# Optimization experiments

Hardware: AMD Instinct MI355X
Metric: run time of the kernel (lower is better)

Reference implementation:

```python
import jax, jax.numpy as jnp
import numpy as np
from jax import lax

H = 256        # HIDDEN_DIM
H2 = 2 * H     # BiLSTM output dim
L = 100        # MAX_SENTENCE_LENGHT
B = 16
WE = 100       # word embed size
PE = 50        # pos embed size
VOC = 46       # POS_VOCAB_SIZE + 1
IN0 = WE + PE  # lstm layer-0 input dim


def setup_inputs():
    key = jax.random.key(0)
    ks = jax.random.split(key, 20)
    s = 0.05
    inp = {}
    inp["word_embeds"] = jax.random.normal(ks[0], (B, L, WE), jnp.float32)
    inp["pos_idx"] = jax.random.randint(ks[1], (B, L), 0, VOC)
    inp["sen_lens"] = jax.random.randint(ks[2], (B,), 1, L + 1)
    inp["pos_emb"] = jax.random.normal(ks[3], (VOC, PE), jnp.float32) * s
    # LSTM layer 0 (input dim 150), directions stacked on axis 0 (fwd, rev)
    inp["w_ih0"] = jax.random.normal(ks[4], (2, 4 * H, IN0), jnp.float32) * s
    inp["w_hh0"] = jax.random.normal(ks[5], (2, 4 * H, H), jnp.float32) * s
    inp["b_ih0"] = jax.random.normal(ks[6], (2, 4 * H), jnp.float32) * s
    inp["b_hh0"] = jax.random.normal(ks[7], (2, 4 * H), jnp.float32) * s
    # LSTM layers 1-3 (input dim 512): [layer, dir, ...]
    inp["w_ih"] = jax.random.normal(ks[8], (3, 2, 4 * H, H2), jnp.float32) * s
    inp["w_hh"] = jax.random.normal(ks[9], (3, 2, 4 * H, H), jnp.float32) * s
    inp["b_ih"] = jax.random.normal(ks[10], (3, 2, 4 * H), jnp.float32) * s
    inp["b_hh"] = jax.random.normal(ks[11], (3, 2, 4 * H), jnp.float32) * s
    # PosTagFC: Linear(1024,512), Linear(512,128), Linear(128,1)
    inp["W1"] = jax.random.normal(ks[12], (H2, 2 * H2), jnp.float32) * s
    inp["b1"] = jax.random.normal(ks[13], (H2,), jnp.float32) * s
    inp["W2"] = jax.random.normal(ks[14], (H // 2, H2), jnp.float32) * s
    inp["b2"] = jax.random.normal(ks[15], (H // 2,), jnp.float32) * s
    inp["W3"] = jax.random.normal(ks[16], (1, H // 2), jnp.float32) * s
    inp["b3"] = jax.random.normal(ks[17], (1,), jnp.float32) * s
    return inp


def _lstm_dir(x, wi, wh, bi, bh, reverse):
    # x: [B, L, F]; PyTorch gate order i, f, g, o
    gx = jnp.einsum('blf,gf->blg', x, wi) + bi + bh  # [B, L, 4H]
    xs = jnp.swapaxes(gx, 0, 1)                      # [L, B, 4H]
    if reverse:
        xs = xs[::-1]
    h0 = jnp.zeros((x.shape[0], H), x.dtype)
    def step(carry, g):
        h, c = carry
        g = g + h @ wh.T
        i, f, gg, o = jnp.split(g, 4, axis=-1)
        c = jax.nn.sigmoid(f) * c + jax.nn.sigmoid(i) * jnp.tanh(gg)
        h = jax.nn.sigmoid(o) * jnp.tanh(c)
        return (h, c), h
    _, hs = lax.scan(step, (h0, h0), xs)
    hs = jnp.swapaxes(hs, 0, 1)                      # [B, L, H]
    if reverse:
        hs = hs[:, ::-1]
    return hs


def _forward(word_embeds, pos_idx, sen_lens, pos_emb,
             w_ih0, w_hh0, b_ih0, b_hh0, w_ih, w_hh, b_ih, b_hh,
             W1, b1, W2, b2, W3, b3):
    x = jnp.concatenate([word_embeds, pos_emb[pos_idx]], axis=2)  # [B, L, 150]
    # 4-layer bidirectional LSTM (eval mode: inter-layer dropout off)
    fwd = _lstm_dir(x, w_ih0[0], w_hh0[0], b_ih0[0], b_hh0[0], False)
    bwd = _lstm_dir(x, w_ih0[1], w_hh0[1], b_ih0[1], b_hh0[1], True)
    x = jnp.concatenate([fwd, bwd], axis=-1)
    for l in range(3):
        fwd = _lstm_dir(x, w_ih[l, 0], w_hh[l, 0], b_ih[l, 0], b_hh[l, 0], False)
        bwd = _lstm_dir(x, w_ih[l, 1], w_hh[l, 1], b_ih[l, 1], b_hh[l, 1], True)
        x = jnp.concatenate([fwd, bwd], axis=-1)  # [B, L, 512]
    lstm_out = x
    # pairwise scoring: split W1 so we never materialize the 1024-dim concat
    rooted = jnp.concatenate([jnp.zeros((B, 1, H2), x.dtype), lstm_out], axis=1)  # [B, L+1, 512]
    W1a, W1b = W1[:, :H2], W1[:, H2:]
    h_first = lstm_out @ W1a.T          # [B, L, 512]
    h_root = rooted @ W1b.T             # [B, L+1, 512]
    h1 = jax.nn.relu(h_first[:, :, None, :] + h_root[:, None, :, :] + b1)  # [B, L, L+1, 512]
    h2 = jax.nn.relu(h1 @ W2.T + b2)    # [B, L, L+1, 128]
    sc = (h2 @ W3.T + b3)[..., 0]       # [B, L, L+1]
    # fill_diagonal_ on the [N,1] fc output zeroes only element 0 -> (0,0)
    sc = sc.at[:, 0, 0].set(0.0)
    row_ok = jnp.arange(L)[None, :] < sen_lens[:, None]        # [B, L]
    col_ok = jnp.arange(L + 1)[None, :] <= sen_lens[:, None]   # [B, L+1]
    sc = jnp.where(row_ok[:, :, None] & col_ok[:, None, :], sc, 0.0)
    return jnp.pad(sc, ((0, 0), (0, 1), (0, 0)))  # [B, 101, 101]


def reference(word_embeds, pos_idx, sen_lens, pos_emb,
              w_ih0, w_hh0, b_ih0, b_hh0, w_ih, w_hh, b_ih, b_hh,
              W1, b1, W2, b2, W3, b3):
    return _forward(word_embeds, pos_idx, sen_lens, pos_emb,
                    w_ih0, w_hh0, b_ih0, b_hh0, w_ih, w_hh, b_ih, b_hh,
                    W1, b1, W2, b2, W3, b3)
```

## Files before the change

### kernel.cpp

```cpp
#include <hip/hip_runtime.h>
#include <stdint.h>

#define NB 16
#define NL 100
#define NOUT (16*101*101)

typedef _Float16 f16x8 __attribute__((ext_vector_type(8)));
typedef float f32x4 __attribute__((ext_vector_type(4)));

__device__ __forceinline__ float sigm(float x) {
    x = fminf(fmaxf(x, -30.f), 30.f);
    return 1.f / (1.f + __expf(-x));
}
__device__ __forceinline__ float tanh_(float x) {
    x = fminf(fmaxf(x, -15.f), 15.f);
    float t = __expf(2.f * x);
    return (t - 1.f) / (t + 1.f);
}
__device__ __forceinline__ uint32_t pack2h(_Float16 a, _Float16 b) {
    return (uint32_t)__builtin_bit_cast(uint16_t, a) |
           ((uint32_t)__builtin_bit_cast(uint16_t, b) << 16);
}


__global__ __launch_bounds__(256) void pack_whh_mfma(const float* __restrict__ w_hh0,
                                                     const float* __restrict__ w_hh,
                                                     uint32_t* __restrict__ wpk) {
    int idx = blockIdx.x * 256 + threadIdx.x;
    if (idx >= 262144) return;
    int l6 = idx & 63;
    int kc = (idx >> 6) & 7;
    int mt = (idx >> 9) & 63;
    int ld = idx >> 15;
    int layer = ld >> 1, d = ld & 1;
    int row = mt * 16 + (l6 & 15);
    int k0 = kc * 32 + (l6 >> 4) * 8;
    const float* src = (layer == 0)
        ? &w_hh0[((size_t)d * 1024 + row) * 256]
        : &w_hh[(((size_t)(layer - 1) * 2 + d) * 1024 + row) * 256];
    uint4 o;
    o.x = pack2h((_Float16)src[k0 + 0], (_Float16)src[k0 + 1]);
    o.y = pack2h((_Float16)src[k0 + 2], (_Float16)src[k0 + 3]);
    o.z = pack2h((_Float16)src[k0 + 4], (_Float16)src[k0 + 5]);
    o.w = pack2h((_Float16)src[k0 + 6], (_Float16)src[k0 + 7]);
    *(uint4*)&wpk[(size_t)idx * 4] = o;
}

__global__ __launch_bounds__(256) void pack_w2_mfma(const float* __restrict__ W2,
                                                    uint32_t* __restrict__ w2pk) {
    int idx = blockIdx.x * 256 + threadIdx.x;
    if (idx >= 16384) return;
    int l6 = idx & 63;
    int nt = (idx >> 6) & 7;
    int sp = (idx >> 9) & 1;
    int kc = idx >> 10;
    int ch = nt * 16 + (l6 & 15);
    int k0 = kc * 32 + (l6 >> 4) * 8;
    uint32_t dw[4];
#pragma unroll
    for (int dwi = 0; dwi < 4; ++dwi) {
        float x0 = W2[(size_t)ch * 512 + k0 + dwi * 2 + 0];
        float x1 = W2[(size_t)ch * 512 + k0 + dwi * 2 + 1];
        _Float16 h0 = (_Float16)x0, h1 = (_Float16)x1;
        _Float16 v0 = sp ? (_Float16)(x0 - (float)h0) : h0;
        _Float16 v1 = sp ? (_Float16)(x1 - (float)h1) : h1;
        dw[dwi] = pack2h(v0, v1);
    }
    *(uint4*)&w2pk[(size_t)idx * 4] = make_uint4(dw[0], dw[1], dw[2], dw[3]);
}

__global__ __launch_bounds__(256) void pack_wi0(const float* __restrict__ w_ih0,
                                                float* __restrict__ wi0p) {
    int idx = blockIdx.x * 256 + threadIdx.x;
    if (idx >= 2 * 1024 * 160) return;
    int k = idx % 160;
    int g = (idx / 160) & 1023;
    int d = idx / (160 * 1024);
    float v = (k < 150) ? w_ih0[((size_t)d * 1024 + g) * 150 + k] : 0.f;
    wi0p[idx] = v;
}

__global__ __launch_bounds__(256) void pack_bias(const float* __restrict__ b_ih0,
                                                 const float* __restrict__ b_hh0,
                                                 const float* __restrict__ b_ih,
                                                 const float* __restrict__ b_hh,
                                                 float* __restrict__ biasp) {
    int idx = blockIdx.x * 256 + threadIdx.x;
    if (idx >= 8 * 1024) return;
    int g = idx & 1023;
    int ld = idx >> 10;
    int l = ld >> 1, d = ld & 1;
    float v;
    if (l == 0) v = b_ih0[d * 1024 + g] + b_hh0[d * 1024 + g];
    else {
        size_t o = ((size_t)(l - 1) * 2 + d) * 1024 + g;
        v = b_ih[o] + b_hh[o];
    }
    biasp[idx] = v;
}

__global__ __launch_bounds__(256) void concat_x0(const float* __restrict__ we,
                                                 const int* __restrict__ pos_idx,
                                                 const float* __restrict__ pos_emb,
                                                 float* __restrict__ x0p) {
    int idx = blockIdx.x * 256 + threadIdx.x;
    if (idx >= 1600 * 160) return;
    int m = idx / 160, k = idx % 160;
    float v;
    if (k < 100) v = we[(size_t)m * 100 + k];
    else if (k < 150) v = pos_emb[(size_t)pos_idx[m] * 50 + (k - 100)];
    else v = 0.f;
    x0p[idx] = v;
}

__global__ __launch_bounds__(256) void zero_out(float* __restrict__ out) {
    int idx = blockIdx.x * 256 + threadIdx.x;
    if (idx < NOUT) out[idx] = 0.f;
}

__global__ __launch_bounds__(256) void gemm_xwT(const float* __restrict__ X,
                                                const float* __restrict__ W,
                                                const float* __restrict__ bias,
                                                float* __restrict__ C,
                                                int K, int ldx, int ldw, int ldc, int coff) {
    __shared__ float As[16][68];
    __shared__ float Bs[16][68];
    const int t = threadIdx.x;
    const int m0 = blockIdx.x * 64, n0 = blockIdx.y * 64;
    const int lr = t >> 2, lc = (t & 3) * 4;
    const int tm = (t & 15) * 4, tn = (t >> 4) * 4;
    float acc[4][4] = {};
    for (int kc = 0; kc < K; kc += 16) {
        float4 av = *(const float4*)&X[(size_t)(m0 + lr) * ldx + kc + lc];
        float4 bv = *(const float4*)&W[(size_t)(n0 + lr) * ldw + kc + lc];
        __syncthreads();
        As[lc + 0][lr] = av.x; As[lc + 1][lr] = av.y; As[lc + 2][lr] = av.z; As[lc + 3][lr] = av.w;
        Bs[lc + 0][lr] = bv.x; Bs[lc + 1][lr] = bv.y; Bs[lc + 2][lr] = bv.z; Bs[lc + 3][lr] = bv.w;
        __syncthreads();
#pragma unroll
        for (int k = 0; k < 16; ++k) {
            float4 a = *(const float4*)&As[k][tm];
            float4 b = *(const float4*)&Bs[k][tn];
            acc[0][0] = fmaf(a.x, b.x, acc[0][0]);
            acc[0][1] = fmaf(a.x, b.y, acc[0][1]);
            acc[0][2] = fmaf(a.x, b.z, acc[0][2]);
            acc[0][3] = fmaf(a.x, b.w, acc[0][3]);
            acc[1][0] = fmaf(a.y, b.x, acc[1][0]);
            acc[1][1] = fmaf(a.y, b.y, acc[1][1]);
            acc[1][2] = fmaf(a.y, b.z, acc[1][2]);
            acc[1][3] = fmaf(a.y, b.w, acc[1][3]);
            acc[2][0] = fmaf(a.z, b.x, acc[2][0]);
            acc[2][1] = fmaf(a.z, b.y, acc[2][1]);
            acc[2][2] = fmaf(a.z, b.z, acc[2][2]);
            acc[2][3] = fmaf(a.z, b.w, acc[2][3]);
            acc[3][0] = fmaf(a.w, b.x, acc[3][0]);
            acc[3][1] = fmaf(a.w, b.y, acc[3][1]);
            acc[3][2] = fmaf(a.w, b.z, acc[3][2]);
            acc[3][3] = fmaf(a.w, b.w, acc[3][3]);
        }
    }
#pragma unroll
    for (int r = 0; r < 4; ++r) {
#pragma unroll
        for (int c = 0; c < 4; ++c) {
            float v = acc[r][c];
            if (bias) v += bias[n0 + tn + c];
            C[(size_t)(m0 + tm + r) * ldc + coff + n0 + tn + c] = v;
        }
    }
}

__global__ __launch_bounds__(1024, 4) void lstm_mfma(const float* __restrict__ gx,
                                                     const uint32_t* __restrict__ wpk_layer,
                                                     float* __restrict__ xout) {
    extern __shared__ uint32_t smem[];
    uint32_t* wtail = smem;
    float*    gbuf  = (float*)(smem + 36864);
    uint32_t* hsta  = smem + 37888;

    const int d = blockIdx.x >> 4;
    const int b = blockIdx.x & 15;
    const int t = threadIdx.x;
    const int w = t >> 6;
    const int l = t & 63;
    const int cgrp = l >> 4;

    uint4 wreg[23];
    const uint32_t* wsrc = wpk_layer + (((size_t)d * 64 + w * 4) * 8) * 256;
#pragma unroll
    for (int mtl = 0; mtl < 4; ++mtl)
#pragma unroll
        for (int kc = 0; kc < 8; ++kc) {
            int f = mtl * 8 + kc;
            uint4 v = *(const uint4*)&wsrc[((size_t)mtl * 8 + kc) * 256 + l * 4];
            if (f < 23) wreg[f] = v;
            else *(uint4*)&wtail[((w * 9 + (f - 23)) * 64 + l) * 4] = v;
        }
    if (t < 128) hsta[t] = 0u;
    float creg = 0.f;
    float gxi = 0.f, gxf = 0.f, gxg = 0.f, gxo = 0.f;
    const float* gxb = gx + ((size_t)d * 1600 + b * 100) * 1024;
    if (t < 256) {
        int tt0 = d ? NL - 1 : 0;
        gxi = gxb[(size_t)tt0 * 1024 + t];
        gxf = gxb[(size_t)tt0 * 1024 + 256 + t];
        gxg = gxb[(size_t)tt0 * 1024 + 512 + t];
        gxo = gxb[(size_t)tt0 * 1024 + 768 + t];
    }
    __syncthreads();

    for (int s = 0; s < NL; ++s) {
        const int tt = d ? (NL - 1 - s) : s;
        f32x4 acc0 = {0.f, 0.f, 0.f, 0.f};
        f32x4 acc1 = {0.f, 0.f, 0.f, 0.f};
        f32x4 acc2 = {0.f, 0.f, 0.f, 0.f};
        f32x4 acc3 = {0.f, 0.f, 0.f, 0.f};
#pragma unroll
        for (int kc = 0; kc < 8; ++kc) {
            uint4 braw = *(const uint4*)&hsta[kc * 16 + cgrp * 4];
            f16x8 B = __builtin_bit_cast(f16x8, braw);
            acc0 = __builtin_amdgcn_mfma_f32_16x16x32_f16(
                __builtin_bit_cast(f16x8, wreg[kc]), B, acc0, 0, 0, 0);
            acc1 = __builtin_amdgcn_mfma_f32_16x16x32_f16(
                __builtin_bit_cast(f16x8, wreg[8 + kc]), B, acc1, 0, 0, 0);
            uint4 a2raw = (kc < 7) ? wreg[16 + kc]
                                   : *(const uint4*)&wtail[((w * 9 + 0) * 64 + l) * 4];
            acc2 = __builtin_amdgcn_mfma_f32_16x16x32_f16(
                __builtin_bit_cast(f16x8, a2raw), B, acc2, 0, 0, 0);
            uint4 a3raw = *(const uint4*)&wtail[((w * 9 + kc + 1) * 64 + l) * 4];
            acc3 = __builtin_amdgcn_mfma_f32_16x16x32_f16(
                __builtin_bit_cast(f16x8, a3raw), B, acc3, 0, 0, 0);
        }
        if ((l & 15) == 0) {
            *(f32x4*)&gbuf[w * 64 +  0 + cgrp * 4] = acc0;
            *(f32x4*)&gbuf[w * 64 + 16 + cgrp * 4] = acc1;
            *(f32x4*)&gbuf[w * 64 + 32 + cgrp * 4] = acc2;
            *(f32x4*)&gbuf[w * 64 + 48 + cgrp * 4] = acc3;
        }
        __syncthreads();
        if (t < 256) {
            float gi = gbuf[t] + gxi;
            float gf = gbuf[256 + t] + gxf;
            float gg = gbuf[512 + t] + gxg;
            float go = gbuf[768 + t] + gxo;
            float cn = fmaf(sigm(gf), creg, sigm(gi) * tanh_(gg));
            creg = cn;
            float hn = sigm(go) * tanh_(cn);
            ((_Float16*)hsta)[t] = (_Float16)hn;
            xout[((size_t)b * NL + tt) * 512 + d * 256 + t] = hn;
            if (s + 1 < NL) {
                int tn = d ? (NL - 2 - s) : (s + 1);
                gxi = gxb[(size_t)tn * 1024 + t];
                gxf = gxb[(size_t)tn * 1024 + 256 + t];
                gxg = gxb[(size_t)tn * 1024 + 512 + t];
                gxo = gxb[(size_t)tn * 1024 + 768 + t];
            }
        }
        __syncthreads();
    }
}

__global__ __launch_bounds__(256) void scorer_mfma(const float* __restrict__ hfr,
                                                   const uint32_t* __restrict__ w2pk,
                                                   const float* __restrict__ b1,
                                                   const float* __restrict__ b2,
                                                   const float* __restrict__ W3,
                                                   const float* __restrict__ b3,
                                                   const int* __restrict__ sen_lens,
                                                   float* __restrict__ out) {
    extern __shared__ uint32_t smem[];
    float*    hfs = (float*)smem;
    float*    hrs = hfs + 16 * 520;
    float*    b1s = hrs + 8 * 520;
    uint32_t* w2s = (uint32_t*)(b1s + 512);

    const int t = threadIdx.x;
    const int wv = t >> 6, l = t & 63;
    const int cgrp = l >> 4;
    const int b = blockIdx.z;
    const int i0 = blockIdx.x * 16;
    const int j0 = blockIdx.y * 8;

#pragma unroll
    for (int rep = 0; rep < 8; ++rep) {
        int slot = rep * 256 + t;
        int row = slot >> 7, c4 = slot & 127;
        int i = i0 + row;
        float4 v = make_float4(0.f, 0.f, 0.f, 0.f);
        if (i < 100) v = *(const float4*)&hfr[((size_t)b * 100 + i) * 1024 + c4 * 4];
        *(float4*)&hfs[row * 520 + c4 * 4] = v;
    }
#pragma unroll
    for (int rep = 0; rep < 4; ++rep) {
        int slot = rep * 256 + t;
        int row = slot >> 7, c4 = slot & 127;
        int j = j0 + row;
        float4 v = make_float4(0.f, 0.f, 0.f, 0.f);
        if (j >= 1 && j <= 100)
            v = *(const float4*)&hfr[((size_t)b * 100 + (j - 1)) * 1024 + 512 + c4 * 4];
        *(float4*)&hrs[row * 520 + c4 * 4] = v;
    }
    if (t < 128) *(float4*)&b1s[t * 4] = *(const float4*)&b1[t * 4];

    float b2r[8], w3r[8];
#pragma unroll
    for (int nt = 0; nt < 8; ++nt) {
        b2r[nt] = b2[nt * 16 + (l & 15)];
        w3r[nt] = W3[nt * 16 + (l & 15)];
    }
    f32x4 accA[8], accB[8];
#pragma unroll
    for (int nt = 0; nt < 8; ++nt) {
        accA[nt] = (f32x4){0.f, 0.f, 0.f, 0.f};
        accB[nt] = (f32x4){0.f, 0.f, 0.f, 0.f};
    }
    const int p0 = (wv * 2) * 16 + (l & 15);
    const int p1 = (wv * 2 + 1) * 16 + (l & 15);
    const int ilA = p0 >> 3, jlA = p0 & 7;
    const int ilB = p1 >> 3, jlB = p1 & 7;
    __syncthreads();

    for (int kc = 0; kc < 16; ++kc) {
#pragma unroll
        for (int rep = 0; rep < 4; ++rep) {
            int slot = rep * 256 + t;
            *(uint4*)&w2s[slot * 4] = *(const uint4*)&w2pk[((size_t)kc * 1024 + slot) * 4];
        }
        __syncthreads();
        const int k0 = kc * 32 + cgrp * 8;
        f16x8 ahi0, alo0, ahi1, alo1;
        {
            const float* hf = &hfs[ilA * 520 + k0];
            const float* hr = &hrs[jlA * 520 + k0];
            const float* bb = &b1s[k0];
#pragma unroll
            for (int j = 0; j < 8; ++j) {
                float v = fmaxf(hf[j] + hr[j] + bb[j], 0.f);
                _Float16 hi = (_Float16)v;
                ahi0[j] = hi;
                alo0[j] = (_Float16)(v - (float)hi);
            }
        }
        {
            const float* hf = &hfs[ilB * 520 + k0];
            const float* hr = &hrs[jlB * 520 + k0];
            const float* bb = &b1s[k0];
#pragma unroll
            for (int j = 0; j < 8; ++j) {
                float v = fmaxf(hf[j] + hr[j] + bb[j], 0.f);
                _Float16 hi = (_Float16)v;
                ahi1[j] = hi;
                alo1[j] = (_Float16)(v - (float)hi);
            }
        }
#pragma unroll
        for (int nt = 0; nt < 8; ++nt) {
            f16x8 bhi = __builtin_bit_cast(f16x8, *(const uint4*)&w2s[((0 * 8 + nt) * 64 + l) * 4]);
            f16x8 blo = __builtin_bit_cast(f16x8, *(const uint4*)&w2s[((1 * 8 + nt) * 64 + l) * 4]);
            accA[nt] = __builtin_amdgcn_mfma_f32_16x16x32_f16(ahi0, bhi, accA[nt], 0, 0, 0);
            accA[nt] = __builtin_amdgcn_mfma_f32_16x16x32_f16(ahi0, blo, accA[nt], 0, 0, 0);
            accA[nt] = __builtin_amdgcn_mfma_f32_16x16x32_f16(alo0, bhi, accA[nt], 0, 0, 0);
            accB[nt] = __builtin_amdgcn_mfma_f32_16x16x32_f16(ahi1, bhi, accB[nt], 0, 0, 0);
            accB[nt] = __builtin_amdgcn_mfma_f32_16x16x32_f16(ahi1, blo, accB[nt], 0, 0, 0);
            accB[nt] = __builtin_amdgcn_mfma_f32_16x16x32_f16(alo1, bhi, accB[nt], 0, 0, 0);
        }
        __syncthreads();
    }
    float sp0[4] = {0.f, 0.f, 0.f, 0.f};
    float sp1[4] = {0.f, 0.f, 0.f, 0.f};
#pragma unroll
    for (int nt = 0; nt < 8; ++nt)
#pragma unroll
        for (int r = 0; r < 4; ++r) {
            sp0[r] += fmaxf(accA[nt][r] + b2r[nt], 0.f) * w3r[nt];
            sp1[r] += fmaxf(accB[nt][r] + b2r[nt], 0.f) * w3r[nt];
        }
#pragma unroll
    for (int r = 0; r < 4; ++r) {
#pragma unroll
        for (int off = 1; off < 16; off <<= 1) {
            sp0[r] += __shfl_xor(sp0[r], off);
            sp1[r] += __shfl_xor(sp1[r], off);
        }
    }
    if ((l & 15) == 0) {
        float bias3 = b3[0];
        int sl = sen_lens[b];
#pragma unroll
        for (int mtl = 0; mtl < 2; ++mtl)
#pragma unroll
            for (int r = 0; r < 4; ++r) {
                int p = (wv * 2 + mtl) * 16 + cgrp * 4 + r;
                int i = i0 + (p >> 3), j = j0 + (p & 7);
                if (i < 100 && j < 101) {
                    float v = (mtl == 0 ? sp0[r] : sp1[r]) + bias3;
                    if (!((i < sl) && (j <= sl)) || (i == 0 && j == 0)) v = 0.f;
                    out[((size_t)b * 101 + i) * 101 + j] = v;
                }
            }
    }
}

extern "C" void kernel_launch(void* const* d_in, const int* in_sizes, int n_in,
                              void* d_out, int out_size, void* d_ws, size_t ws_size,
                              hipStream_t stream) {
    const float* we       = (const float*)d_in[0];
    const int*   pos_idx  = (const int*)d_in[1];
    const int*   sen_lens = (const int*)d_in[2];
    const float* pos_emb  = (const float*)d_in[3];
    const float* w_ih0    = (const float*)d_in[4];
    const float* w_hh0    = (const float*)d_in[5];
    const float* b_ih0    = (const float*)d_in[6];
    const float* b_hh0    = (const float*)d_in[7];
    const float* w_ih     = (const float*)d_in[8];
    const float* w_hh     = (const float*)d_in[9];
    const float* b_ih     = (const float*)d_in[10];
    const float* b_hh     = (const float*)d_in[11];
    const float* W1       = (const float*)d_in[12];
    const float* b1       = (const float*)d_in[13];
    const float* W2       = (const float*)d_in[14];
    const float* b2       = (const float*)d_in[15];
    const float* W3       = (const float*)d_in[16];
    const float* b3       = (const float*)d_in[17];
    float* out = (float*)d_out;

    float* ws    = (float*)d_ws;
    float* x0p   = ws;
    float* gx    = x0p + 256000;
    float* xA    = gx + 3276800;
    float* xB    = xA + 819200;
    float* hfr   = xB + 819200;
    float* wi0p  = hfr + 1638400;
    float* biasp = wi0p + 327680;
    uint32_t* wpk  = (uint32_t*)(biasp + 8192);
    uint32_t* w2pk = wpk + 1048576;

    pack_whh_mfma<<<1024, 256, 0, stream>>>(w_hh0, w_hh, wpk);
    pack_w2_mfma<<<64, 256, 0, stream>>>(W2, w2pk);
    pack_wi0<<<1280, 256, 0, stream>>>(w_ih0, wi0p);
    pack_bias<<<32, 256, 0, stream>>>(b_ih0, b_hh0, b_ih, b_hh, biasp);
    concat_x0<<<1000, 256, 0, stream>>>(we, pos_idx, pos_emb, x0p);

    const int LSTM_SMEM = 38016 * 4;
    const int SCOR_SMEM = 68352;

    for (int d = 0; d < 2; ++d)
        gemm_xwT<<<dim3(25, 16), 256, 0, stream>>>(
            x0p, wi0p + (size_t)d * 1024 * 160, biasp + d * 1024,
            gx + (size_t)d * 1600 * 1024, 160, 160, 160, 1024, 0);
    lstm_mfma<<<32, 1024, LSTM_SMEM, stream>>>(gx, wpk, xA);

    const float* xin = xA;
    float* xo = xB;
    for (int l = 1; l < 4; ++l) {
        for (int d = 0; d < 2; ++d)
            gemm_xwT<<<dim3(25, 16), 256, 0, stream>>>(
                xin, w_ih + (((size_t)(l - 1) * 2 + d) * 1024) * 512,
                biasp + (l * 2 + d) * 1024,
                gx + (size_t)d * 1600 * 1024, 512, 512, 512, 1024, 0);
        lstm_mfma<<<32, 1024, LSTM_SMEM, stream>>>(gx, wpk + (size_t)l * 262144, xo);
        float* tmp = (float*)xin; xin = xo; xo = tmp;
    }
    const float* lstm_out = xin;

    gemm_xwT<<<dim3(25, 8), 256, 0, stream>>>(lstm_out, W1, nullptr, hfr,
                                              512, 512, 1024, 1024, 0);
    gemm_xwT<<<dim3(25, 8), 256, 0, stream>>>(lstm_out, W1 + 512, nullptr, hfr,
                                              512, 512, 1024, 1024, 512);

    zero_out<<<(NOUT + 255) / 256, 256, 0, stream>>>(out);
    scorer_mfma<<<dim3(7, 13, 16), 256, SCOR_SMEM, stream>>>(hfr, w2pk, b1, b2, W3, b3,
                                                             sen_lens, out);
}
```

Baseline: 1.205 ms.

## Restructure LSTM recurrence so each wave owns full gate sets; stream W2 from global

```diff
diff --git a/kernel.cpp b/kernel.cpp
--- a/kernel.cpp
+++ b/kernel.cpp
@@ -21,6 +21,8 @@
     return (uint32_t)__builtin_bit_cast(uint16_t, a) |
            ((uint32_t)__builtin_bit_cast(uint16_t, b) << 16);
 }
+#define MFMA16(A, B, C) __builtin_amdgcn_mfma_f32_16x16x32_f16( \
+    __builtin_bit_cast(f16x8, A), (B), (C), 0, 0, 0)
 
 
 __global__ __launch_bounds__(256) void pack_whh_mfma(const float* __restrict__ w_hh0,
@@ -170,109 +172,134 @@
     }
 }
 
-__global__ __launch_bounds__(1024, 4) void lstm_mfma(const float* __restrict__ gx,
-                                                     const uint32_t* __restrict__ wpk_layer,
-                                                     float* __restrict__ xout) {
-    extern __shared__ uint32_t smem[];
-    uint32_t* wtail = smem;
-    float*    gbuf  = (float*)(smem + 36864);
-    uint32_t* hsta  = smem + 37888;
-
+__global__ __launch_bounds__(512, 2) void lstm_v5(const float* __restrict__ gx,
+                                                  const uint32_t* __restrict__ wpk_layer,
+                                                  float* __restrict__ xout) {
+    __shared__ uint32_t hs2[256];
     const int d = blockIdx.x >> 4;
     const int b = blockIdx.x & 15;
     const int t = threadIdx.x;
     const int w = t >> 6;
     const int l = t & 63;
-    const int cgrp = l >> 4;
-
-    uint4 wreg[23];
-    const uint32_t* wsrc = wpk_layer + (((size_t)d * 64 + w * 4) * 8) * 256;
-#pragma unroll
-    for (int mtl = 0; mtl < 4; ++mtl)
-#pragma unroll
-        for (int kc = 0; kc < 8; ++kc) {
-            int f = mtl * 8 + kc;
-            uint4 v = *(const uint4*)&wsrc[((size_t)mtl * 8 + kc) * 256 + l * 4];
-            if (f < 23) wreg[f] = v;
-            else *(uint4*)&wtail[((w * 9 + (f - 23)) * 64 + l) * 4] = v;
-        }
-    if (t < 128) hsta[t] = 0u;
-    float creg = 0.f;
-    float gxi = 0.f, gxf = 0.f, gxg = 0.f, gxo = 0.f;
+    const int lg = l >> 4;
+
+    const uint32_t* wb = wpk_layer + (size_t)d * 131072;
+#define WFRAG(mt, kc) (*(const uint4*)&wb[(((mt) * 8 + (kc)) * 64 + l) * 4])
+
+    uint4 wr0[16], wr1[16];
+#pragma unroll
+    for (int kc = 0; kc < 8; ++kc) {
+#pragma unroll
+        for (int s = 0; s < 2; ++s) {
+            wr0[kc * 2 + s] = WFRAG(w * 2 + s, kc);
+            wr1[kc * 2 + s] = WFRAG(16 + w * 2 + s, kc);
+        }
+    }
+    if (t < 128) hs2[t] = 0u;
+    f32x4 c0 = {0.f, 0.f, 0.f, 0.f}, c1 = {0.f, 0.f, 0.f, 0.f};
+    __syncthreads();
+
     const float* gxb = gx + ((size_t)d * 1600 + b * 100) * 1024;
-    if (t < 256) {
-        int tt0 = d ? NL - 1 : 0;
-        gxi = gxb[(size_t)tt0 * 1024 + t];
-        gxf = gxb[(size_t)tt0 * 1024 + 256 + t];
-        gxg = gxb[(size_t)tt0 * 1024 + 512 + t];
-        gxo = gxb[(size_t)tt0 * 1024 + 768 + t];
-    }
-    __syncthreads();
-
+    const int gxoff = w * 32 + lg * 4;
+
+#pragma unroll 1
     for (int s = 0; s < NL; ++s) {
         const int tt = d ? (NL - 1 - s) : s;
-        f32x4 acc0 = {0.f, 0.f, 0.f, 0.f};
-        f32x4 acc1 = {0.f, 0.f, 0.f, 0.f};
-        f32x4 acc2 = {0.f, 0.f, 0.f, 0.f};
-        f32x4 acc3 = {0.f, 0.f, 0.f, 0.f};
+        const uint32_t* hc = hs2 + (s & 1) * 128;
+        uint32_t* hn = hs2 + ((s + 1) & 1) * 128;
+
+        f32x4 a00 = {0.f,0.f,0.f,0.f}, a01 = {0.f,0.f,0.f,0.f};
+        f32x4 a10 = {0.f,0.f,0.f,0.f}, a11 = {0.f,0.f,0.f,0.f};
+        f32x4 a20 = {0.f,0.f,0.f,0.f}, a21 = {0.f,0.f,0.f,0.f};
+        f32x4 a30 = {0.f,0.f,0.f,0.f}, a31 = {0.f,0.f,0.f,0.f};
+
+        uint4 sr[2][4];
+#pragma unroll
+        for (int p = 0; p < 2; ++p) {
+            sr[p][0] = WFRAG(32 + w * 2 + 0, p);
+            sr[p][1] = WFRAG(32 + w * 2 + 1, p);
+            sr[p][2] = WFRAG(48 + w * 2 + 0, p);
+            sr[p][3] = WFRAG(48 + w * 2 + 1, p);
+        }
+        f32x4 gxv[8];
+
 #pragma unroll
         for (int kc = 0; kc < 8; ++kc) {
-            uint4 braw = *(const uint4*)&hsta[kc * 16 + cgrp * 4];
+            uint4 braw = *(const uint4*)&hc[kc * 16 + lg * 4];
             f16x8 B = __builtin_bit_cast(f16x8, braw);
-            acc0 = __builtin_amdgcn_mfma_f32_16x16x32_f16(
-                __builtin_bit_cast(f16x8, wreg[kc]), B, acc0, 0, 0, 0);
-            acc1 = __builtin_amdgcn_mfma_f32_16x16x32_f16(
-                __builtin_bit_cast(f16x8, wreg[8 + kc]), B, acc1, 0, 0, 0);
-            uint4 a2raw = (kc < 7) ? wreg[16 + kc]
-                                   : *(const uint4*)&wtail[((w * 9 + 0) * 64 + l) * 4];
-            acc2 = __builtin_amdgcn_mfma_f32_16x16x32_f16(
-                __builtin_bit_cast(f16x8, a2raw), B, acc2, 0, 0, 0);
-            uint4 a3raw = *(const uint4*)&wtail[((w * 9 + kc + 1) * 64 + l) * 4];
-            acc3 = __builtin_amdgcn_mfma_f32_16x16x32_f16(
-                __builtin_bit_cast(f16x8, a3raw), B, acc3, 0, 0, 0);
+            a00 = MFMA16(wr0[kc * 2 + 0], B, a00);
+            a01 = MFMA16(wr0[kc * 2 + 1], B, a01);
+            a10 = MFMA16(wr1[kc * 2 + 0], B, a10);
+            a11 = MFMA16(wr1[kc * 2 + 1], B, a11);
+            uint4 s0 = sr[kc & 1][0], s1 = sr[kc & 1][1];
+            uint4 s2 = sr[kc & 1][2], s3 = sr[kc & 1][3];
+            if (kc < 6) {
+                const int p = kc + 2;
+                sr[kc & 1][0] = WFRAG(32 + w * 2 + 0, p);
+                sr[kc & 1][1] = WFRAG(32 + w * 2 + 1, p);
+                sr[kc & 1][2] = WFRAG(48 + w * 2 + 0, p);
+                sr[kc & 1][3] = WFRAG(48 + w * 2 + 1, p);
+            }
+            if (kc == 6) {
+#pragma unroll
+                for (int g = 0; g < 4; ++g)
+#pragma unroll
+                    for (int si = 0; si < 2; ++si)
+                        gxv[g * 2 + si] = *(const f32x4*)&gxb[(size_t)tt * 1024 +
+                                                              g * 256 + si * 16 + gxoff];
+            }
+            a20 = MFMA16(s0, B, a20);
+            a21 = MFMA16(s1, B, a21);
+            a30 = MFMA16(s2, B, a30);
+            a31 = MFMA16(s3, B, a31);
+        }
+
+        float h0[4], h1[4];
+#pragma unroll
+        for (int r = 0; r < 4; ++r) {
+            float gi = a00[r] + gxv[0][r];
+            float gf = a10[r] + gxv[2][r];
+            float gg = a20[r] + gxv[4][r];
+            float go = a30[r] + gxv[6][r];
+            float cn = fmaf(sigm(gf), c0[r], sigm(gi) * tanh_(gg));
+            c0[r] = cn;
+            h0[r] = sigm(go) * tanh_(cn);
+            gi = a01[r] + gxv[1][r];
+            gf = a11[r] + gxv[3][r];
+            gg = a21[r] + gxv[5][r];
+            go = a31[r] + gxv[7][r];
+            cn = fmaf(sigm(gf), c1[r], sigm(gi) * tanh_(gg));
+            c1[r] = cn;
+            h1[r] = sigm(go) * tanh_(cn);
         }
         if ((l & 15) == 0) {
-            *(f32x4*)&gbuf[w * 64 +  0 + cgrp * 4] = acc0;
-            *(f32x4*)&gbuf[w * 64 + 16 + cgrp * 4] = acc1;
-            *(f32x4*)&gbuf[w * 64 + 32 + cgrp * 4] = acc2;
-            *(f32x4*)&gbuf[w * 64 + 48 + cgrp * 4] = acc3;
+            const int u0 = w * 32 + lg * 4;
+            uint2 p0, p1;
+            p0.x = pack2h((_Float16)h0[0], (_Float16)h0[1]);
+            p0.y = pack2h((_Float16)h0[2], (_Float16)h0[3]);
+            p1.x = pack2h((_Float16)h1[0], (_Float16)h1[1]);
+            p1.y = pack2h((_Float16)h1[2], (_Float16)h1[3]);
+            *(uint2*)((char*)hn + (size_t)u0 * 2) = p0;
+            *(uint2*)((char*)hn + (size_t)(u0 + 16) * 2) = p1;
+            float* xo = &xout[((size_t)b * NL + tt) * 512 + d * 256 + u0];
+            *(float4*)xo = make_float4(h0[0], h0[1], h0[2], h0[3]);
+            *(float4*)(xo + 16) = make_float4(h1[0], h1[1], h1[2], h1[3]);
         }
         __syncthreads();
-        if (t < 256) {
-            float gi = gbuf[t] + gxi;
-            float gf = gbuf[256 + t] + gxf;
-            float gg = gbuf[512 + t] + gxg;
-            float go = gbuf[768 + t] + gxo;
-            float cn = fmaf(sigm(gf), creg, sigm(gi) * tanh_(gg));
-            creg = cn;
-            float hn = sigm(go) * tanh_(cn);
-            ((_Float16*)hsta)[t] = (_Float16)hn;
-            xout[((size_t)b * NL + tt) * 512 + d * 256 + t] = hn;
-            if (s + 1 < NL) {
-                int tn = d ? (NL - 2 - s) : (s + 1);
-                gxi = gxb[(size_t)tn * 1024 + t];
-                gxf = gxb[(size_t)tn * 1024 + 256 + t];
-                gxg = gxb[(size_t)tn * 1024 + 512 + t];
-                gxo = gxb[(size_t)tn * 1024 + 768 + t];
-            }
-        }
-        __syncthreads();
-    }
-}
-
-__global__ __launch_bounds__(256) void scorer_mfma(const float* __restrict__ hfr,
-                                                   const uint32_t* __restrict__ w2pk,
-                                                   const float* __restrict__ b1,
-                                                   const float* __restrict__ b2,
-                                                   const float* __restrict__ W3,
-                                                   const float* __restrict__ b3,
-                                                   const int* __restrict__ sen_lens,
-                                                   float* __restrict__ out) {
-    extern __shared__ uint32_t smem[];
-    float*    hfs = (float*)smem;
-    float*    hrs = hfs + 16 * 520;
-    float*    b1s = hrs + 8 * 520;
-    uint32_t* w2s = (uint32_t*)(b1s + 512);
+    }
+#undef WFRAG
+}
+
+__global__ __launch_bounds__(256) void scorer_v2(const float* __restrict__ hfr,
+                                                 const uint32_t* __restrict__ w2pk,
+                                                 const float* __restrict__ b1,
+                                                 const float* __restrict__ b2,
+                                                 const float* __restrict__ W3,
+                                                 const float* __restrict__ b3,
+                                                 const int* __restrict__ sen_lens,
+                                                 float* __restrict__ out) {
+    __shared__ float hfs[16][520];
+    __shared__ float hrs[8][520];
 
     const int t = threadIdx.x;
     const int wv = t >> 6, l = t & 63;
@@ -288,19 +315,20 @@
         int i = i0 + row;
         float4 v = make_float4(0.f, 0.f, 0.f, 0.f);
         if (i < 100) v = *(const float4*)&hfr[((size_t)b * 100 + i) * 1024 + c4 * 4];
-        *(float4*)&hfs[row * 520 + c4 * 4] = v;
+        *(float4*)&hfs[row][c4 * 4] = v;
     }
 #pragma unroll
     for (int rep = 0; rep < 4; ++rep) {
         int slot = rep * 256 + t;
         int row = slot >> 7, c4 = slot & 127;
         int j = j0 + row;
+        float4 bv = *(const float4*)&b1[c4 * 4];
         float4 v = make_float4(0.f, 0.f, 0.f, 0.f);
         if (j >= 1 && j <= 100)
             v = *(const float4*)&hfr[((size_t)b * 100 + (j - 1)) * 1024 + 512 + c4 * 4];
-        *(float4*)&hrs[row * 520 + c4 * 4] = v;
-    }
-    if (t < 128) *(float4*)&b1s[t * 4] = *(const float4*)&b1[t * 4];
+        v.x += bv.x; v.y += bv.y; v.z += bv.z; v.w += bv.w;
+        *(float4*)&hrs[row][c4 * 4] = v;
+    }
 
     float b2r[8], w3r[8];
 #pragma unroll
@@ -321,42 +349,44 @@
     __syncthreads();
 
     for (int kc = 0; kc < 16; ++kc) {
-#pragma unroll
-        for (int rep = 0; rep < 4; ++rep) {
-            int slot = rep * 256 + t;
-            *(uint4*)&w2s[slot * 4] = *(const uint4*)&w2pk[((size_t)kc * 1024 + slot) * 4];
-        }
-        __syncthreads();
         const int k0 = kc * 32 + cgrp * 8;
         f16x8 ahi0, alo0, ahi1, alo1;
         {
-            const float* hf = &hfs[ilA * 520 + k0];
-            const float* hr = &hrs[jlA * 520 + k0];
-            const float* bb = &b1s[k0];
-#pragma unroll
-            for (int j = 0; j < 8; ++j) {
-                float v = fmaxf(hf[j] + hr[j] + bb[j], 0.f);
+            f32x4 f0 = *(const f32x4*)&hfs[ilA][k0];
+            f32x4 f1 = *(const f32x4*)&hfs[ilA][k0 + 4];
+            f32x4 r0 = *(const f32x4*)&hrs[jlA][k0];
+            f32x4 r1 = *(const f32x4*)&hrs[jlA][k0 + 4];
+#pragma unroll
+            for (int j = 0; j < 4; ++j) {
+                float v = fmaxf(f0[j] + r0[j], 0.f);
                 _Float16 hi = (_Float16)v;
-                ahi0[j] = hi;
-                alo0[j] = (_Float16)(v - (float)hi);
+                ahi0[j] = hi; alo0[j] = (_Float16)(v - (float)hi);
+                v = fmaxf(f1[j] + r1[j], 0.f);
+                hi = (_Float16)v;
+                ahi0[4 + j] = hi; alo0[4 + j] = (_Float16)(v - (float)hi);
             }
         }
         {
-            const float* hf = &hfs[ilB * 520 + k0];
-            const float* hr = &hrs[jlB * 520 + k0];
-            const float* bb = &b1s[k0];
-#pragma unroll
-            for (int j = 0; j < 8; ++j) {
-                float v = fmaxf(hf[j] + hr[j] + bb[j], 0.f);
+            f32x4 f0 = *(const f32x4*)&hfs[ilB][k0];
+            f32x4 f1 = *(const f32x4*)&hfs[ilB][k0 + 4];
+            f32x4 r0 = *(const f32x4*)&hrs[jlB][k0];
+            f32x4 r1 = *(const f32x4*)&hrs[jlB][k0 + 4];
+#pragma unroll
+            for (int j = 0; j < 4; ++j) {
+                float v = fmaxf(f0[j] + r0[j], 0.f);
                 _Float16 hi = (_Float16)v;
-                ahi1[j] = hi;
-                alo1[j] = (_Float16)(v - (float)hi);
+                ahi1[j] = hi; alo1[j] = (_Float16)(v - (float)hi);
+                v = fmaxf(f1[j] + r1[j], 0.f);
+                hi = (_Float16)v;
+                ahi1[4 + j] = hi; alo1[4 + j] = (_Float16)(v - (float)hi);
             }
         }
 #pragma unroll
         for (int nt = 0; nt < 8; ++nt) {
-            f16x8 bhi = __builtin_bit_cast(f16x8, *(const uint4*)&w2s[((0 * 8 + nt) * 64 + l) * 4]);
-            f16x8 blo = __builtin_bit_cast(f16x8, *(const uint4*)&w2s[((1 * 8 + nt) * 64 + l) * 4]);
+            f16x8 bhi = __builtin_bit_cast(f16x8,
+                *(const uint4*)&w2pk[((((size_t)kc * 2 + 0) * 8 + nt) * 64 + l) * 4]);
+            f16x8 blo = __builtin_bit_cast(f16x8,
+                *(const uint4*)&w2pk[((((size_t)kc * 2 + 1) * 8 + nt) * 64 + l) * 4]);
             accA[nt] = __builtin_amdgcn_mfma_f32_16x16x32_f16(ahi0, bhi, accA[nt], 0, 0, 0);
             accA[nt] = __builtin_amdgcn_mfma_f32_16x16x32_f16(ahi0, blo, accA[nt], 0, 0, 0);
             accA[nt] = __builtin_amdgcn_mfma_f32_16x16x32_f16(alo0, bhi, accA[nt], 0, 0, 0);
@@ -364,7 +394,6 @@
             accB[nt] = __builtin_amdgcn_mfma_f32_16x16x32_f16(ahi1, blo, accB[nt], 0, 0, 0);
             accB[nt] = __builtin_amdgcn_mfma_f32_16x16x32_f16(alo1, bhi, accB[nt], 0, 0, 0);
         }
-        __syncthreads();
     }
     float sp0[4] = {0.f, 0.f, 0.f, 0.f};
     float sp1[4] = {0.f, 0.f, 0.f, 0.f};
@@ -441,14 +470,11 @@
     pack_bias<<<32, 256, 0, stream>>>(b_ih0, b_hh0, b_ih, b_hh, biasp);
     concat_x0<<<1000, 256, 0, stream>>>(we, pos_idx, pos_emb, x0p);
 
-    const int LSTM_SMEM = 38016 * 4;
-    const int SCOR_SMEM = 68352;
-
     for (int d = 0; d < 2; ++d)
         gemm_xwT<<<dim3(25, 16), 256, 0, stream>>>(
             x0p, wi0p + (size_t)d * 1024 * 160, biasp + d * 1024,
             gx + (size_t)d * 1600 * 1024, 160, 160, 160, 1024, 0);
-    lstm_mfma<<<32, 1024, LSTM_SMEM, stream>>>(gx, wpk, xA);
+    lstm_v5<<<32, 512, 0, stream>>>(gx, wpk, xA);
 
     const float* xin = xA;
     float* xo = xB;
@@ -458,7 +484,7 @@
                 xin, w_ih + (((size_t)(l - 1) * 2 + d) * 1024) * 512,
                 biasp + (l * 2 + d) * 1024,
                 gx + (size_t)d * 1600 * 1024, 512, 512, 512, 1024, 0);
-        lstm_mfma<<<32, 1024, LSTM_SMEM, stream>>>(gx, wpk + (size_t)l * 262144, xo);
+        lstm_v5<<<32, 512, 0, stream>>>(gx, wpk + (size_t)l * 262144, xo);
         float* tmp = (float*)xin; xin = xo; xo = tmp;
     }
     const float* lstm_out = xin;
@@ -469,6 +495,6 @@
                                               512, 512, 1024, 1024, 512);
 
     zero_out<<<(NOUT + 255) / 256, 256, 0, stream>>>(out);
-    scorer_mfma<<<dim3(7, 13, 16), 256, SCOR_SMEM, stream>>>(hfr, w2pk, b1, b2, W3, b3,
-                                                             sen_lens, out);
-}
+    scorer_v2<<<dim3(7, 13, 16), 256, 0, stream>>>(hfr, w2pk, b1, b2, W3, b3,
+                                                   sen_lens, out);
+}
```

After: 4.144 ms. 3.44x slower.
